# Kernel optimization log

Measured on AMD Instinct MI355X. Metric: run time of the kernel, lower is better.

Reference implementation:

```python
import jax, jax.numpy as jnp
import numpy as np

IN_SIZE = 1024
HID = 2048
OUT = 1024
M_STEPS = 100   # max extra ponder steps -> up to M_STEPS+1 total steps
EPS = 0.01


def setup_inputs() -> dict:
    key = jax.random.key(0)
    ks = jax.random.split(key, 11)
    inv = 1.0 / np.sqrt(HID)

    def unif(k, shape, scale):
        return jax.random.uniform(k, shape, jnp.float32, -scale, scale)

    return {
        "x": jax.random.normal(ks[0], (IN_SIZE,), jnp.float32),
        "h0": jax.random.normal(ks[1], (HID,), jnp.float32) * 0.1,
        "c0": jax.random.normal(ks[2], (HID,), jnp.float32) * 0.1,
        "W_ih": unif(ks[3], (4 * HID, 1 + IN_SIZE), inv),
        "b_ih": unif(ks[4], (4 * HID,), inv),
        "W_hh": unif(ks[5], (4 * HID, HID), inv),
        "b_hh": unif(ks[6], (4 * HID,), inv),
        "w_halt": unif(ks[7], (HID,), inv),
        "b_halt": jnp.ones((1,), jnp.float32),  # fc_halt.bias = 1.0 per source
        "W_out": unif(ks[8], (OUT, HID), inv),
        "b_out": unif(ks[9], (OUT,), inv),
    }


def reference(x, h0, c0, W_ih, b_ih, W_hh, b_hh, w_halt, b_halt, W_out, b_out):
    # Input contribution is constant across steps except the prepended halt flag
    # (1 on first step, 0 after). Precompute it once.
    ih_x = W_ih[:, 1:] @ x + b_ih + b_hh      # (4H,)
    w_flag = W_ih[:, 0]                        # (4H,)

    def step(carry, flag):
        h, c = carry
        gates = ih_x + flag * w_flag + W_hh @ h  # (4H,)
        i, f, g, o = jnp.split(gates, 4)
        i = jax.nn.sigmoid(i)
        f = jax.nn.sigmoid(f)
        g = jnp.tanh(g)
        o = jax.nn.sigmoid(o)
        c = f * c + i * g
        h = o * jnp.tanh(c)
        return (h, c), (h, c)

    flags = jnp.concatenate(
        [jnp.ones((1,), x.dtype), jnp.zeros((M_STEPS,), x.dtype)])
    _, (H, C) = jax.lax.scan(step, (h0, c0), flags)  # (M+1, HID) each

    p = jax.nn.sigmoid(H @ w_halt + b_halt[0])       # (M+1,) halting probs
    csum = jnp.cumsum(p)
    halted = csum >= 1.0 - EPS
    # n = first step where cumulative halt prob crosses threshold, capped at M
    n = jnp.where(jnp.any(halted), jnp.argmax(halted), M_STEPS)
    # remainder r = 1 - sum(p[:n]); csum[n] - p[n] == sum(p[:n])
    r = 1.0 - jnp.where(n > 0, csum[n] - p[n], 0.0)

    idx = jnp.arange(M_STEPS + 1)
    w = jnp.where(idx < n, p, jnp.where(idx == n, r, 0.0))  # (M+1,)

    outputs = H @ W_out.T + b_out                    # (M+1, OUT)
    output = w @ outputs                             # (OUT,) weights sum to 1
    h_out = w @ H                                    # (HID,)
    c_out = w @ C                                    # (HID,)
    ponder = n.astype(x.dtype) + 1.0 + r
    return output, (h_out, c_out), ponder
```

## Files before the change

kernel.cpp:

```cpp
#include <hip/hip_runtime.h>


#define HID    2048
#define INS    1024
#define OUTS   1024
#define MSTEPS 100
#define NBLK   256
#define NTHR   512
#define NWAVE  8
#define JPB    8
#define RPB    32
#define SLOTF  16

typedef unsigned long long u64;
typedef unsigned int u32;

__device__ __forceinline__ float wave_allreduce(float v) {
    #pragma unroll
    for (int off = 32; off > 0; off >>= 1)
        v += __shfl_xor(v, off, 64);
    return v;
}

__device__ __forceinline__ u64 pack_tag(unsigned tag, float v) {
    return ((u64)tag << 32) | (u64)__float_as_uint(v);
}
__device__ __forceinline__ u64 aload(const u64* p) {
    return __hip_atomic_load(p, __ATOMIC_RELAXED, __HIP_MEMORY_SCOPE_AGENT);
}
__device__ __forceinline__ void astore(u64* p, u64 v) {
    __hip_atomic_store(p, v, __ATOMIC_RELAXED, __HIP_MEMORY_SCOPE_AGENT);
}


__global__
__attribute__((amdgpu_flat_work_group_size(NTHR, NTHR)))
__attribute__((amdgpu_waves_per_eu(2, 2)))
void alstm_kernel(
    const float* __restrict__ x,      const float* __restrict__ h0,
    const float* __restrict__ c0,     const float* __restrict__ W_ih,
    const float* __restrict__ b_ih,   const float* __restrict__ W_hh,
    const float* __restrict__ b_hh,   const float* __restrict__ w_halt,
    const float* __restrict__ b_halt, const float* __restrict__ W_out,
    const float* __restrict__ b_out,  float* __restrict__ out,
    float* __restrict__ ws)
{
    const int b    = blockIdx.x;
    const int tid  = threadIdx.x;
    const int wave = tid >> 6;
    const int lane = tid & 63;

    float* arrive = ws;
    float* mail   = ws + NBLK * SLOTF;
    float* hbuf0  = ws + 2 * NBLK * SLOTF;
    float* hbuf1  = hbuf0 + HID;

    __shared__ float x_lds[INS];
    __shared__ float hjoint[HID];
    __shared__ float hcur[HID];
    __shared__ float gate_lds[RPB];
    __shared__ float ihx_lds[RPB];
    __shared__ float red_lds[4];
    __shared__ float bcast_lds;
    __shared__ float psum[NWAVE];

    const int j_own = b * JPB + tid;
    const int lr0   = 4 * wave;
    const int rbase = (lr0 >> 3) * HID + b * JPB + (lr0 & 7);

    #define SYNC_ROUND(tag_, part_, dot_) do {                                 \
        if (tid == 0) {                                                        \
            __threadfence();           \
            astore((u64*)(arrive + SLOTF * b), pack_tag((tag_), (part_)));     \
        }                                                                      \
        if (b == 0) {                                                          \
            float pf = 0.f;                                                    \
            if (tid < NBLK) {                                                  \
                u64 v = aload((u64*)(arrive + SLOTF * tid));                   \
                while ((unsigned)(v >> 32) != (unsigned)(tag_)) {              \
                    __builtin_amdgcn_s_sleep(1);                               \
                    v = aload((u64*)(arrive + SLOTF * tid));                   \
                }                                                              \
                pf = __uint_as_float((unsigned)v);                             \
            }                                                                  \
            float s = wave_allreduce(pf);                                      \
            if (lane == 0 && wave < 4) red_lds[wave] = s;                      \
            __syncthreads();                                                   \
            if (tid == 0)                                                      \
                bcast_lds = red_lds[0] + red_lds[1] + red_lds[2] + red_lds[3]; \
            __syncthreads();                                                   \
            if (tid < NBLK)                                                    \
                astore((u64*)(mail + SLOTF * tid), pack_tag((tag_), bcast_lds)); \
        }                                                                      \
        if (tid == 0) {                                                        \
            u64 v = aload((u64*)(mail + SLOTF * b));                           \
            while ((unsigned)(v >> 32) != (unsigned)(tag_)) {                  \
                __builtin_amdgcn_s_sleep(1);                                   \
                v = aload((u64*)(mail + SLOTF * b));                           \
            }                                                                  \
            bcast_lds = __uint_as_float((unsigned)v);                          \
            __threadfence();        \
        }                                                                      \
        __syncthreads();                                                       \
        (dot_) = bcast_lds;                                                    \
    } while (0)

    #define DOT4(H4P, G0, G1, G2, G3) do {                                     \
        const float4* h4__ = (H4P);                                            \
        _Pragma("unroll")                                                      \
        for (int m = 0; m < 8; ++m) {                                          \
            float4 hh = h4__[lane + 64 * m];                                   \
            G0 += wa0[m].x*hh.x + wa0[m].y*hh.y + wa0[m].z*hh.z + wa0[m].w*hh.w; \
            G1 += wa1[m].x*hh.x + wa1[m].y*hh.y + wa1[m].z*hh.z + wa1[m].w*hh.w; \
            G2 += wa2[m].x*hh.x + wa2[m].y*hh.y + wa2[m].z*hh.z + wa2[m].w*hh.w; \
            G3 += wa3[m].x*hh.x + wa3[m].y*hh.y + wa3[m].z*hh.z + wa3[m].w*hh.w; \
        }                                                                      \
    } while (0)

    const float bh = b_halt[0];
    float2 xv  = ((const float2*)x)[tid];
    float4 h0v = ((const float4*)h0)[tid];
    float c_reg = (tid < JPB) ? c0[j_own]     : 0.f;
    float whv   = (tid < JPB) ? w_halt[j_own] : 0.f;
    float bo    = (tid < 4)   ? b_out[b * 4 + tid] : 0.f;
    float bsum = 0.f, wflg = 0.f;
    if (lane < 4) {
        const int lr = lr0 + lane;
        const int r  = (lr >> 3) * HID + b * JPB + (lr & 7);
        bsum = b_ih[r] + b_hh[r];
        wflg = W_ih[(size_t)r * (INS + 1)];
    }
    __builtin_amdgcn_sched_barrier(0);

    const float*  wr_[4];
    const float4* wv_[4];
    int p0_[4];
    #pragma unroll
    for (int rr = 0; rr < 4; ++rr) {
        const int lr = lr0 + rr;
        const int r  = (lr >> 3) * HID + b * JPB + (lr & 7);
        wr_[rr] = W_ih + (size_t)r * (INS + 1) + 1;
        p0_[rr] = (4 - ((r + 1) & 3)) & 3;
        wv_[rr] = (const float4*)(wr_[rr] + p0_[rr]);
    }
    float4 iw0[4], iw1[4], iw2[4], iw3[4];
    #pragma unroll
    for (int ii = 0; ii < 4; ++ii) {
        const int i  = lane + 64 * ii;
        const int ic = (i < 255) ? i : 0;
        iw0[ii] = wv_[0][ic];
        iw1[ii] = wv_[1][ic];
        iw2[ii] = wv_[2][ic];
        iw3[ii] = wv_[3][ic];
    }
    __builtin_amdgcn_sched_barrier(0);

    float4 wa0[8], wa1[8], wa2[8], wa3[8];
    {
        const float4* s0 = (const float4*)(W_hh + (size_t)(rbase + 0) * HID);
        const float4* s1 = (const float4*)(W_hh + (size_t)(rbase + 1) * HID);
        const float4* s2 = (const float4*)(W_hh + (size_t)(rbase + 2) * HID);
        const float4* s3 = (const float4*)(W_hh + (size_t)(rbase + 3) * HID);
        #pragma unroll
        for (int m = 0; m < 8; ++m) {
            wa0[m] = s0[lane + 64 * m];
            wa1[m] = s1[lane + 64 * m];
            wa2[m] = s2[lane + 64 * m];
            wa3[m] = s3[lane + 64 * m];
        }
    }
    __builtin_amdgcn_sched_barrier(0);

    const int orow  = b * 4 + (wave & 3);
    const int ohalf = wave >> 2;
    const float4* wrow = (const float4*)(W_out + (size_t)orow * HID) + ohalf * 256;
    float4 wo0 = wrow[lane], wo1 = wrow[lane + 64],
           wo2 = wrow[lane + 128], wo3 = wrow[lane + 192];
    __builtin_amdgcn_sched_barrier(0);

    ((float2*)x_lds)[tid]  = xv;
    ((float4*)hjoint)[tid] = h0v;
    __syncthreads();

    float a0 = 0.f, a1 = 0.f, a2 = 0.f, a3 = 0.f;
    #pragma unroll
    for (int ii = 0; ii < 4; ++ii) {
        const int   i   = lane + 64 * ii;
        const int   ic  = (i < 255) ? i : 0;
        const float msk = (i < 255) ? 1.f : 0.f;
        #pragma unroll
        for (int rr = 0; rr < 4; ++rr) {
            float4 w4 = (rr == 0) ? iw0[ii] : (rr == 1) ? iw1[ii]
                      : (rr == 2) ? iw2[ii] : iw3[ii];
            const int k = p0_[rr] + 4 * ic;
            float s = w4.x * x_lds[k]     + w4.y * x_lds[k + 1]
                    + w4.z * x_lds[k + 2] + w4.w * x_lds[k + 3];
            s *= msk;
            if      (rr == 0) a0 += s;
            else if (rr == 1) a1 += s;
            else if (rr == 2) a2 += s;
            else              a3 += s;
        }
    }
    if (lane < 4) {
        #pragma unroll
        for (int rr = 0; rr < 4; ++rr) {
            const int p0 = p0_[rr];
            const int e  = (lane < p0) ? lane : 1020 + lane;
            float s = wr_[rr][e] * x_lds[e];
            if      (rr == 0) a0 += s;
            else if (rr == 1) a1 += s;
            else if (rr == 2) a2 += s;
            else              a3 += s;
        }
    }

    float g0 = 0.f, g1 = 0.f, g2 = 0.f, g3 = 0.f;
    DOT4((const float4*)hjoint, g0, g1, g2, g3);

    a0 = wave_allreduce(a0); a1 = wave_allreduce(a1);
    a2 = wave_allreduce(a2); a3 = wave_allreduce(a3);
    g0 = wave_allreduce(g0); g1 = wave_allreduce(g1);
    g2 = wave_allreduce(g2); g3 = wave_allreduce(g3);
    if (lane < 4) {
        float av = (lane == 0) ? a0 : (lane == 1) ? a1 : (lane == 2) ? a2 : a3;
        float gv = (lane == 0) ? g0 : (lane == 1) ? g1 : (lane == 2) ? g2 : g3;
        ihx_lds[lr0 + lane]  = av + bsum;
        gate_lds[lr0 + lane] = av + bsum + wflg + gv;
    }
    __syncthreads();
    ((float4*)hjoint)[tid] = make_float4(0.f, 0.f, 0.f, 0.f);

    float h_reg = 0.f, cbar = 0.f;
    float csum = 0.f, r_halt = 0.f;
    int   n_halt = 0;
    for (int t = 0; t <= MSTEPS; ++t) {
        float part = 0.f;
        float* hdst = (t & 1) ? hbuf1 : hbuf0;
        if (tid < JPB) {
            float iv = gate_lds[0 * JPB + tid];
            float fv = gate_lds[1 * JPB + tid];
            float gv = gate_lds[2 * JPB + tid];
            float ov = gate_lds[3 * JPB + tid];
            iv = 1.f / (1.f + expf(-iv));
            fv = 1.f / (1.f + expf(-fv));
            gv = tanhf(gv);
            ov = 1.f / (1.f + expf(-ov));
            c_reg = fv * c_reg + iv * gv;
            h_reg = ov * tanhf(c_reg);
            hdst[j_own] = h_reg;
            part = h_reg * whv;
        }
        part += __shfl_down(part, 4, 64);
        part += __shfl_down(part, 2, 64);
        part += __shfl_down(part, 1, 64);

        float dotv;
        SYNC_ROUND(t + 1, part, dotv);

        float p = 1.f / (1.f + expf(-(dotv + bh)));
        float prev = csum;
        csum += p;
        bool  halt_now = (csum >= 1.f - 0.01f) || (t == MSTEPS);
        float wt = halt_now ? (1.f - prev) : p;

        float4 hv = ((const float4*)hdst)[tid];
        float4 hb = ((float4*)hjoint)[tid];
        hb.x += wt * hv.x; hb.y += wt * hv.y;
        hb.z += wt * hv.z; hb.w += wt * hv.w;
        ((float4*)hjoint)[tid] = hb;
        if (tid < JPB) cbar += wt * c_reg;
        if (halt_now) { n_halt = t; r_halt = 1.f - prev; break; }

        ((float4*)hcur)[tid] = hv;
        __syncthreads();

        {
            float m0 = 0.f, m1 = 0.f, m2 = 0.f, m3 = 0.f;
            DOT4((const float4*)hcur, m0, m1, m2, m3);
            m0 = wave_allreduce(m0); m1 = wave_allreduce(m1);
            m2 = wave_allreduce(m2); m3 = wave_allreduce(m3);
            if (lane < 4) {
                float mv = (lane == 0) ? m0 : (lane == 1) ? m1
                         : (lane == 2) ? m2 : m3;
                gate_lds[lr0 + lane] = ihx_lds[lr0 + lane] + mv;
            }
        }
        __syncthreads();
    }

    __syncthreads();
    if (tid < JPB) {
        out[OUTS + j_own]       = hjoint[j_own];
        out[OUTS + HID + j_own] = cbar;
    }
    if (b == 0 && tid == 0) out[OUTS + 2 * HID] = (float)(n_halt + 1) + r_halt;

    {
        const float4* hb4 = (const float4*)hjoint + ohalf * 256;
        float acc = 0.f;
        { float4 h4 = hb4[lane];       acc += wo0.x*h4.x + wo0.y*h4.y + wo0.z*h4.z + wo0.w*h4.w; }
        { float4 h4 = hb4[lane + 64];  acc += wo1.x*h4.x + wo1.y*h4.y + wo1.z*h4.z + wo1.w*h4.w; }
        { float4 h4 = hb4[lane + 128]; acc += wo2.x*h4.x + wo2.y*h4.y + wo2.z*h4.z + wo2.w*h4.w; }
        { float4 h4 = hb4[lane + 192]; acc += wo3.x*h4.x + wo3.y*h4.y + wo3.z*h4.z + wo3.w*h4.w; }
        acc = wave_allreduce(acc);
        if (lane == 0) psum[wave] = acc;
    }
    __syncthreads();
    if (tid < 4) out[b * 4 + tid] = psum[tid] + psum[tid + 4] + bo;

    #undef SYNC_ROUND
    #undef DOT4
}

extern "C" void kernel_launch(void* const* d_in, const int* in_sizes, int n_in,
                              void* d_out, int out_size, void* d_ws, size_t ws_size,
                              hipStream_t stream) {
    const float* x      = (const float*)d_in[0];
    const float* h0     = (const float*)d_in[1];
    const float* c0     = (const float*)d_in[2];
    const float* W_ih   = (const float*)d_in[3];
    const float* b_ih   = (const float*)d_in[4];
    const float* W_hh   = (const float*)d_in[5];
    const float* b_hh   = (const float*)d_in[6];
    const float* w_halt = (const float*)d_in[7];
    const float* b_halt = (const float*)d_in[8];
    const float* W_out  = (const float*)d_in[9];
    const float* b_out  = (const float*)d_in[10];
    float* out = (float*)d_out;
    float* ws  = (float*)d_ws;

    hipMemsetAsync(d_ws, 0, 32768, stream);

    alstm_kernel<<<dim3(NBLK), dim3(NTHR), 0, stream>>>(
        x, h0, c0, W_ih, b_ih, W_hh, b_hh, w_halt, b_halt, W_out, b_out,
        out, ws);
}
```

Before: 167.8 us.

## Replace gather-broadcast halt reduction with flat all-to-all barrier and local halt dot

The two-hop grid sync (every block reports a partial halt dot to block 0, which reduces and mails back) is replaced by a flat barrier: each block publishes a step counter, and every block polls all 256 counters itself. Each block then reads the full new hidden state and computes the halt probability dot product locally, removing the serial round-trip through block 0. The weighted hidden accumulator now stays in registers rather than LDS. The cost is 256 polling loads per block per step, plus a redundant 2048-element halt dot in every block. Correctness depends on relaxed atomics combined with a vmcnt wait for ordering instead of threadfences.

```diff
diff --git a/kernel.cpp b/kernel.cpp
--- a/kernel.cpp
+++ b/kernel.cpp
@@ -22,13 +22,13 @@
     return v;
 }
 
-__device__ __forceinline__ u64 pack_tag(unsigned tag, float v) {
-    return ((u64)tag << 32) | (u64)__float_as_uint(v);
-}
 __device__ __forceinline__ u64 aload(const u64* p) {
     return __hip_atomic_load(p, __ATOMIC_RELAXED, __HIP_MEMORY_SCOPE_AGENT);
 }
 __device__ __forceinline__ void astore(u64* p, u64 v) {
+    __hip_atomic_store(p, v, __ATOMIC_RELAXED, __HIP_MEMORY_SCOPE_AGENT);
+}
+__device__ __forceinline__ void astoref(float* p, float v) {
     __hip_atomic_store(p, v, __ATOMIC_RELAXED, __HIP_MEMORY_SCOPE_AGENT);
 }
 
@@ -51,8 +51,7 @@
     const int lane = tid & 63;
 
     float* arrive = ws;
-    float* mail   = ws + NBLK * SLOTF;
-    float* hbuf0  = ws + 2 * NBLK * SLOTF;
+    float* hbuf0  = ws + NBLK * SLOTF;
     float* hbuf1  = hbuf0 + HID;
 
     __shared__ float x_lds[INS];
@@ -60,50 +59,11 @@
     __shared__ float hcur[HID];
     __shared__ float gate_lds[RPB];
     __shared__ float ihx_lds[RPB];
-    __shared__ float red_lds[4];
-    __shared__ float bcast_lds;
     __shared__ float psum[NWAVE];
 
     const int j_own = b * JPB + tid;
     const int lr0   = 4 * wave;
     const int rbase = (lr0 >> 3) * HID + b * JPB + (lr0 & 7);
-
-    #define SYNC_ROUND(tag_, part_, dot_) do {                                 \
-        if (tid == 0) {                                                        \
-            __threadfence();           \
-            astore((u64*)(arrive + SLOTF * b), pack_tag((tag_), (part_)));     \
-        }                                                                      \
-        if (b == 0) {                                                          \
-            float pf = 0.f;                                                    \
-            if (tid < NBLK) {                                                  \
-                u64 v = aload((u64*)(arrive + SLOTF * tid));                   \
-                while ((unsigned)(v >> 32) != (unsigned)(tag_)) {              \
-                    __builtin_amdgcn_s_sleep(1);                               \
-                    v = aload((u64*)(arrive + SLOTF * tid));                   \
-                }                                                              \
-                pf = __uint_as_float((unsigned)v);                             \
-            }                                                                  \
-            float s = wave_allreduce(pf);                                      \
-            if (lane == 0 && wave < 4) red_lds[wave] = s;                      \
-            __syncthreads();                                                   \
-            if (tid == 0)                                                      \
-                bcast_lds = red_lds[0] + red_lds[1] + red_lds[2] + red_lds[3]; \
-            __syncthreads();                                                   \
-            if (tid < NBLK)                                                    \
-                astore((u64*)(mail + SLOTF * tid), pack_tag((tag_), bcast_lds)); \
-        }                                                                      \
-        if (tid == 0) {                                                        \
-            u64 v = aload((u64*)(mail + SLOTF * b));                           \
-            while ((unsigned)(v >> 32) != (unsigned)(tag_)) {                  \
-                __builtin_amdgcn_s_sleep(1);                                   \
-                v = aload((u64*)(mail + SLOTF * b));                           \
-            }                                                                  \
-            bcast_lds = __uint_as_float((unsigned)v);                          \
-            __threadfence();        \
-        }                                                                      \
-        __syncthreads();                                                       \
-        (dot_) = bcast_lds;                                                    \
-    } while (0)
 
     #define DOT4(H4P, G0, G1, G2, G3) do {                                     \
         const float4* h4__ = (H4P);                                            \
@@ -120,8 +80,8 @@
     const float bh = b_halt[0];
     float2 xv  = ((const float2*)x)[tid];
     float4 h0v = ((const float4*)h0)[tid];
-    float c_reg = (tid < JPB) ? c0[j_own]     : 0.f;
-    float whv   = (tid < JPB) ? w_halt[j_own] : 0.f;
+    float4 wh4 = ((const float4*)w_halt)[tid];
+    float c_reg = (tid < JPB) ? c0[j_own] : 0.f;
     float bo    = (tid < 4)   ? b_out[b * 4 + tid] : 0.f;
     float bsum = 0.f, wflg = 0.f;
     if (lane < 4) {
@@ -229,13 +189,11 @@
         gate_lds[lr0 + lane] = av + bsum + wflg + gv;
     }
     __syncthreads();
-    ((float4*)hjoint)[tid] = make_float4(0.f, 0.f, 0.f, 0.f);
-
-    float h_reg = 0.f, cbar = 0.f;
-    float csum = 0.f, r_halt = 0.f;
-    int   n_halt = 0;
+
+    float4 hb4 = make_float4(0.f, 0.f, 0.f, 0.f);
+    float  h_reg = 0.f, cbar = 0.f, csum = 0.f, r_halt = 0.f;
+    int    n_halt = 0;
     for (int t = 0; t <= MSTEPS; ++t) {
-        float part = 0.f;
         float* hdst = (t & 1) ? hbuf1 : hbuf0;
         if (tid < JPB) {
             float iv = gate_lds[0 * JPB + tid];
@@ -248,32 +206,46 @@
             ov = 1.f / (1.f + expf(-ov));
             c_reg = fv * c_reg + iv * gv;
             h_reg = ov * tanhf(c_reg);
-            hdst[j_own] = h_reg;
-            part = h_reg * whv;
-        }
-        part += __shfl_down(part, 4, 64);
-        part += __shfl_down(part, 2, 64);
-        part += __shfl_down(part, 1, 64);
-
-        float dotv;
-        SYNC_ROUND(t + 1, part, dotv);
-
+            astoref(hdst + j_own, h_reg);
+        }
+        asm volatile("s_waitcnt vmcnt(0)" ::: "memory");
+        if (tid == 0)
+            astore((u64*)(arrive + SLOTF * b), (u64)(t + 1));
+
+        if (tid < NBLK) {
+            const u64* slot = (const u64*)(arrive + SLOTF * tid);
+            u64 v = aload(slot);
+            while (v < (u64)(t + 1)) {
+                __builtin_amdgcn_s_sleep(1);
+                v = aload(slot);
+            }
+        }
+        __syncthreads();
+
+        const u64* hsrc = (const u64*)((t & 1) ? hbuf1 : hbuf0);
+        u64 hA = aload(hsrc + 2 * tid);
+        u64 hB = aload(hsrc + 2 * tid + 1);
+        float4 hv = make_float4(__uint_as_float((u32)hA),
+                                __uint_as_float((u32)(hA >> 32)),
+                                __uint_as_float((u32)hB),
+                                __uint_as_float((u32)(hB >> 32)));
+        ((float4*)hcur)[tid] = hv;
+
+        float part = hv.x * wh4.x + hv.y * wh4.y + hv.z * wh4.z + hv.w * wh4.w;
+        part = wave_allreduce(part);
+        if (lane == 0) psum[wave] = part;
+        __syncthreads();
+        float dotv = ((psum[0] + psum[1]) + (psum[2] + psum[3]))
+                   + ((psum[4] + psum[5]) + (psum[6] + psum[7]));
         float p = 1.f / (1.f + expf(-(dotv + bh)));
         float prev = csum;
         csum += p;
         bool  halt_now = (csum >= 1.f - 0.01f) || (t == MSTEPS);
         float wt = halt_now ? (1.f - prev) : p;
-
-        float4 hv = ((const float4*)hdst)[tid];
-        float4 hb = ((float4*)hjoint)[tid];
-        hb.x += wt * hv.x; hb.y += wt * hv.y;
-        hb.z += wt * hv.z; hb.w += wt * hv.w;
-        ((float4*)hjoint)[tid] = hb;
+        hb4.x += wt * hv.x; hb4.y += wt * hv.y;
+        hb4.z += wt * hv.z; hb4.w += wt * hv.w;
         if (tid < JPB) cbar += wt * c_reg;
         if (halt_now) { n_halt = t; r_halt = 1.f - prev; break; }
-
-        ((float4*)hcur)[tid] = hv;
-        __syncthreads();
 
         {
             float m0 = 0.f, m1 = 0.f, m2 = 0.f, m3 = 0.f;
@@ -289,27 +261,25 @@
         __syncthreads();
     }
 
+    ((float4*)hjoint)[tid] = hb4;
+    if (b == 0) ((float4*)(out + OUTS))[tid] = hb4;
+    if (tid < JPB) out[OUTS + HID + j_own] = cbar;
+    if (b == 0 && tid == 0) out[OUTS + 2 * HID] = (float)(n_halt + 1) + r_halt;
     __syncthreads();
-    if (tid < JPB) {
-        out[OUTS + j_own]       = hjoint[j_own];
-        out[OUTS + HID + j_own] = cbar;
-    }
-    if (b == 0 && tid == 0) out[OUTS + 2 * HID] = (float)(n_halt + 1) + r_halt;
 
     {
-        const float4* hb4 = (const float4*)hjoint + ohalf * 256;
+        const float4* hb4p = (const float4*)hjoint + ohalf * 256;
         float acc = 0.f;
-        { float4 h4 = hb4[lane];       acc += wo0.x*h4.x + wo0.y*h4.y + wo0.z*h4.z + wo0.w*h4.w; }
-        { float4 h4 = hb4[lane + 64];  acc += wo1.x*h4.x + wo1.y*h4.y + wo1.z*h4.z + wo1.w*h4.w; }
-        { float4 h4 = hb4[lane + 128]; acc += wo2.x*h4.x + wo2.y*h4.y + wo2.z*h4.z + wo2.w*h4.w; }
-        { float4 h4 = hb4[lane + 192]; acc += wo3.x*h4.x + wo3.y*h4.y + wo3.z*h4.z + wo3.w*h4.w; }
+        { float4 h4 = hb4p[lane];       acc += wo0.x*h4.x + wo0.y*h4.y + wo0.z*h4.z + wo0.w*h4.w; }
+        { float4 h4 = hb4p[lane + 64];  acc += wo1.x*h4.x + wo1.y*h4.y + wo1.z*h4.z + wo1.w*h4.w; }
+        { float4 h4 = hb4p[lane + 128]; acc += wo2.x*h4.x + wo2.y*h4.y + wo2.z*h4.z + wo2.w*h4.w; }
+        { float4 h4 = hb4p[lane + 192]; acc += wo3.x*h4.x + wo3.y*h4.y + wo3.z*h4.z + wo3.w*h4.w; }
         acc = wave_allreduce(acc);
         if (lane == 0) psum[wave] = acc;
     }
     __syncthreads();
     if (tid < 4) out[b * 4 + tid] = psum[tid] + psum[tid + 4] + bo;
 
-    #undef SYNC_ROUND
     #undef DOT4
 }
 
```

Result: faster. 155.5 us (-7.3%).
